# Optimization experiments

Hardware: AMD Instinct MI355X
Metric: run time of the kernel (lower is better)

## Reference

```python
import jax, jax.numpy as jnp
import numpy as np

B, SQ, SKV, D, H, DH, P = 8, 2048, 2048, 1024, 8, 128, 1024
LN_EPS = 1e-3  # keras LayerNormalization default


def _glorot(key, shape):
    fan_in, fan_out = shape[-2], shape[-1]
    lim = np.sqrt(6.0 / (fan_in + fan_out))
    return jax.random.uniform(key, shape, jnp.float32, -lim, lim)


def _layernorm(x, gamma, beta, eps=LN_EPS):
    mu = jnp.mean(x, axis=-1, keepdims=True)
    var = jnp.mean(jnp.square(x - mu), axis=-1, keepdims=True)
    return (x - mu) * jax.lax.rsqrt(var + eps) * gamma + beta


def setup_inputs() -> dict:
    key = jax.random.key(0)
    ks = jax.random.split(key, 8)
    return {
        "query": jax.random.normal(ks[0], (B, SQ, D), jnp.float32),
        "value": jax.random.normal(ks[1], (B, SKV, D), jnp.float32),
        "W1": _glorot(ks[2], (H, D, DH)),   # per-head query proj (stacked)
        "W2": _glorot(ks[3], (H, D, DH)),   # per-head key proj
        "W3": _glorot(ks[4], (H, D, DH)),   # per-head value proj
        "Wp": _glorot(ks[5], (H * DH, P)),  # output projection
        "bp": jnp.zeros((P,), jnp.float32),
        "Wt": _glorot(ks[6], (P, P)),       # transform (relu FFN)
        "bt": jnp.zeros((P,), jnp.float32),
        "g1": jnp.ones((P,), jnp.float32),
        "b1": jnp.zeros((P,), jnp.float32),
        "g2": jnp.ones((P,), jnp.float32),
        "b2": jnp.zeros((P,), jnp.float32),
    }


def reference(query, value, W1, W2, W3, Wp, bp, Wt, bt, g1, b1, g2, b2):
    # batched multi-head attention (original loops over heads; math identical)
    q = jnp.einsum("bsd,hde->bhse", query, W1)   # [B,H,SQ,DH]
    k = jnp.einsum("btd,hde->bhte", value, W2)   # [B,H,SKV,DH]
    v = jnp.einsum("btd,hde->bhte", value, W3)   # [B,H,SKV,DH]
    scale = 1.0 / jnp.sqrt(jnp.asarray(DH, jnp.float32))
    scores = jnp.einsum("bhse,bhte->bhst", q, k) * scale
    attn = jax.nn.softmax(scores, axis=-1)
    ctx = jnp.einsum("bhst,bhte->bhse", attn, v)  # [B,H,SQ,DH]
    # concat heads along feature axis
    cat = ctx.transpose(0, 2, 1, 3).reshape(B, SQ, H * DH)
    # project + residual + layernorm (dropout inactive: rate=0 / inference)
    proj = cat @ Wp + bp + query
    proj = _layernorm(proj, g1, b1)
    # relu transform + residual + layernorm
    t = jax.nn.relu(proj @ Wt + bt) + proj
    return _layernorm(t, g2, b2)
```

## Files before the change

kernel.cpp:

```cpp
#include <hip/hip_runtime.h>
#include <hip/hip_bf16.h>


typedef __bf16 bf16x8 __attribute__((ext_vector_type(8)));
typedef float  f32x4  __attribute__((ext_vector_type(4)));
typedef float  f32x16 __attribute__((ext_vector_type(16)));
typedef unsigned u32x4 __attribute__((ext_vector_type(4)));

#define GLDS16(g, l)                                                         \
  __builtin_amdgcn_global_load_lds(                                          \
      (__attribute__((address_space(1))) void*)(g),                          \
      (__attribute__((address_space(3))) void*)(l), 16, 0, 0)

__device__ __forceinline__ unsigned short f2bfu(float f) {
  unsigned int u = __builtin_bit_cast(unsigned int, f);
  u += 0x7fffu + ((u >> 16) & 1u);
  return (unsigned short)(u >> 16);
}
__device__ __forceinline__ float bfu2f(unsigned short u) {
  return __builtin_bit_cast(float, (unsigned int)u << 16);
}

__global__ __launch_bounds__(256) void cast2_f32_bf16(
    const float* __restrict__ in0, unsigned short* __restrict__ out0,
    const float* __restrict__ in1, unsigned short* __restrict__ out1, int n) {
  const float* in = blockIdx.z ? in1 : in0;
  unsigned short* out = blockIdx.z ? out1 : out0;
  int i = (blockIdx.x * 256 + threadIdx.x) * 4;
  int stride = gridDim.x * 256 * 4;
  for (; i < n; i += stride) {
    float4 v = *(const float4*)(in + i);
    ushort4 o;
    o.x = f2bfu(v.x); o.y = f2bfu(v.y); o.z = f2bfu(v.z); o.w = f2bfu(v.w);
    *(ushort4*)(out + i) = o;
  }
}

__device__ __forceinline__ void tc_body(const float* in, unsigned short* out,
                                        int R, int C) {
  __shared__ float tile[32][33];
  int tx = threadIdx.x, ty = threadIdx.y;
  int c0 = blockIdx.x * 32, r0 = blockIdx.y * 32;
#pragma unroll
  for (int j = 0; j < 4; j++)
    tile[ty + j * 8][tx] = in[(size_t)(r0 + ty + j * 8) * C + c0 + tx];
  __syncthreads();
#pragma unroll
  for (int j = 0; j < 4; j++)
    out[(size_t)(c0 + ty + j * 8) * R + r0 + tx] = f2bfu(tile[tx][ty + j * 8]);
}

__global__ __launch_bounds__(256) void transpose_heads(
    const float* __restrict__ W1, const float* __restrict__ W2,
    const float* __restrict__ W3, unsigned short* __restrict__ O1,
    unsigned short* __restrict__ O2, unsigned short* __restrict__ O3) {
  int z = blockIdx.z, t = z >> 3, s = z & 7;
  const float* in = (t == 0 ? W1 : t == 1 ? W2 : W3) + (size_t)s * 1024 * 128;
  unsigned short* out = (t == 0 ? O1 : t == 1 ? O2 : O3) + (size_t)s * 1024 * 128;
  tc_body(in, out, 1024, 128);
}

__global__ __launch_bounds__(256) void transpose_sq(
    const float* __restrict__ Wp, const float* __restrict__ Wt,
    unsigned short* __restrict__ Op, unsigned short* __restrict__ Ot) {
  const float* in = blockIdx.z ? Wt : Wp;
  unsigned short* out = blockIdx.z ? Ot : Op;
  tc_body(in, out, 1024, 1024);
}

template <int MODE>
__global__ __launch_bounds__(512, 2) void gemm256(
    const unsigned short* __restrict__ A, const unsigned short* __restrict__ Bt,
    void* __restrict__ out, const float* __restrict__ bias,
    const void* __restrict__ extra, float scale, float scale1,
    long strideA, long strideB, long strideO, int ntiles) {
  int bz = blockIdx.z;
  A  += (size_t)bz * strideA;
  Bt += (size_t)bz * strideB;
  float sc = bz ? scale1 : scale;
  int nb = gridDim.x;
  int qq = nb >> 3;
  int lin = blockIdx.x;
  int sw = (lin & 7) * qq + (lin >> 3);
  int nt = sw % ntiles, mt = sw / ntiles;
  int m0 = mt * 256, n0 = nt * 256;
  int tid = threadIdx.x;
  int wid = tid >> 6, lane = tid & 63;
  int l15 = lane & 15, l4 = lane >> 4;
  int wm = (wid >> 2) * 128, wn = (wid & 3) * 64;

  __shared__ alignas(16) char lds[131072];

  f32x4 acc[8][4];
#pragma unroll
  for (int i = 0; i < 8; i++)
#pragma unroll
    for (int j = 0; j < 4; j++) acc[i][j] = (f32x4){0.f, 0.f, 0.f, 0.f};

  const char* gA = (const char*)A + (size_t)m0 * 2048;
  const char* gB = (const char*)Bt + (size_t)n0 * 2048;

  auto STAGE = [&](int buf, int t) {
    char* ab = lds + buf * 65536;
    char* bb = ab + 32768;
#pragma unroll
    for (int i = 0; i < 4; i++) {
      int s = i * 512 + tid;
      int row = s >> 3;
      int g = (s & 7) ^ (row & 7);
      unsigned dst = (unsigned)((i * 512 + (tid & ~63)) * 16);
      GLDS16(gA + (size_t)row * 2048 + t * 128 + g * 16, ab + dst);
      GLDS16(gB + (size_t)row * 2048 + t * 128 + g * 16, bb + dst);
    }
  };

  STAGE(0, 0);
  for (int t = 0; t < 16; t++) {
    __builtin_amdgcn_sched_barrier(0);
    __builtin_amdgcn_s_barrier();
    if (t < 15) {
      STAGE((t + 1) & 1, t + 1);
      asm volatile("s_waitcnt vmcnt(8)" ::: "memory");
    } else {
      asm volatile("s_waitcnt vmcnt(0)" ::: "memory");
    }
    __builtin_amdgcn_s_barrier();
    __builtin_amdgcn_sched_barrier(0);

    const char* ab = lds + (t & 1) * 65536;
    const char* bb = ab + 32768;
#pragma unroll
    for (int kk = 0; kk < 2; kk++) {
      bf16x8 bfr[4];
#pragma unroll
      for (int nf = 0; nf < 4; nf++) {
        int r = wn + nf * 16 + l15;
        bfr[nf] = *(const bf16x8*)(bb + r * 128 + (((kk * 4 + l4) ^ (r & 7)) << 4));
      }
#pragma unroll
      for (int mh = 0; mh < 2; mh++) {
        bf16x8 af[4];
#pragma unroll
        for (int mf = 0; mf < 4; mf++) {
          int r = wm + mh * 64 + mf * 16 + l15;
          af[mf] = *(const bf16x8*)(ab + r * 128 + (((kk * 4 + l4) ^ (r & 7)) << 4));
        }
        __builtin_amdgcn_s_setprio(1);
#pragma unroll
        for (int mf = 0; mf < 4; mf++)
#pragma unroll
          for (int nf = 0; nf < 4; nf++)
            acc[mh * 4 + mf][nf] = __builtin_amdgcn_mfma_f32_16x16x32_bf16(
                af[mf], bfr[nf], acc[mh * 4 + mf][nf], 0, 0, 0);
        __builtin_amdgcn_s_setprio(0);
      }
    }
  }

  unsigned short* outp = (unsigned short*)out + (size_t)bz * strideO;
#pragma unroll
  for (int mi = 0; mi < 8; mi++)
#pragma unroll
    for (int nf = 0; nf < 4; nf++)
#pragma unroll
      for (int r = 0; r < 4; r++) {
        int gm = m0 + wm + mi * 16 + l4 * 4 + r;
        int gn = n0 + wn + nf * 16 + l15;
        float v = acc[mi][nf][r];
        if constexpr (MODE == 0) {
          int b = gm >> 11, s = gm & 2047, h = gn >> 7, e = gn & 127;
          outp[((((size_t)b * 8 + h) * 2048 + s) << 7) + e] = f2bfu(v * sc);
        } else if constexpr (MODE == 1) {
          outp[(size_t)gm * 2048 + gn] = f2bfu(v);
        } else if constexpr (MODE == 2) {
          float pl = bfu2f(((const unsigned short*)extra)[(size_t)gm * 1024 + gn]);
          outp[(size_t)gm * 1024 + gn] = f2bfu(v + bias[gn] + pl);
        } else {
          float pl = bfu2f(((const unsigned short*)extra)[(size_t)gm * 1024 + gn]);
          outp[(size_t)gm * 1024 + gn] = f2bfu(fmaxf(v + bias[gn], 0.0f) + pl);
        }
      }
}

__global__ __launch_bounds__(512) void fa_kernel(
    const unsigned short* __restrict__ Qh,
    const unsigned short* __restrict__ Kh,
    const unsigned short* __restrict__ Vt,
    unsigned short* __restrict__ catO) {
  int h = blockIdx.x, qt = blockIdx.y, b = blockIdx.z;
  int tid = threadIdx.x, wid = tid >> 6, lane = tid & 63;
  int q31 = lane & 31, hi = lane >> 5;

  __shared__ alignas(16) char lds[131072];

  const char* gK = (const char*)(Kh + (((size_t)b * 8 + h) * 2048) * 128);
  const char* gV = (const char*)(Vt + ((size_t)b * 1024 + h * 128) * 2048);

  bf16x8 qf[8];
  {
    const char* gQ = (const char*)(Qh + (((size_t)b * 8 + h) * 2048
                        + (size_t)qt * 256 + wid * 32 + q31) * 128);
#pragma unroll
    for (int ks = 0; ks < 8; ks++)
      qf[ks] = *(const bf16x8*)(gQ + ks * 32 + hi * 16);
  }

  f32x16 o[4];
#pragma unroll
  for (int et = 0; et < 4; et++)
#pragma unroll
    for (int r = 0; r < 16; r++) o[et][r] = 0.f;
  float lacc0 = 0.f, lacc1 = 0.f;

  auto STAGE_K = [&](int kt) {
    char* kb = lds + (kt & 3) * 16384;
#pragma unroll
    for (int pass = 0; pass < 2; pass++) {
      int c = pass * 512 + tid;
      int row = c >> 4, ch = c & 15;
      int g = ch ^ (row & 15);
      GLDS16(gK + (size_t)(kt * 64 + row) * 256 + g * 16,
             kb + (pass * 512 + (tid & ~63)) * 16);
    }
  };
  auto STAGE_V = [&](int kt) {
    char* vb = lds + 65536 + (kt & 3) * 16384;
#pragma unroll
    for (int pass = 0; pass < 2; pass++) {
      int c = pass * 512 + tid;
      int row = c >> 4, g = c & 15;
      int gp = g ^ (row & 15);
      int e = ((gp >> 3) << 6) + row;
      GLDS16(gV + (size_t)e * 4096 + kt * 128 + (gp & 7) * 16,
             vb + (pass * 512 + (tid & ~63)) * 16);
    }
  };
  auto QK = [&](int kt, f32x16& r0, f32x16& r1) {
    const char* kb = lds + (kt & 3) * 16384;
#pragma unroll
    for (int r = 0; r < 16; r++) { r0[r] = 0.f; r1[r] = 0.f; }
#pragma unroll
    for (int ks = 0; ks < 8; ks++) {
      int g = ((2 * ks + hi) ^ (q31 & 15)) << 4;
      bf16x8 k0 = *(const bf16x8*)(kb + q31 * 256 + g);
      bf16x8 k1 = *(const bf16x8*)(kb + (q31 + 32) * 256 + g);
      r0 = __builtin_amdgcn_mfma_f32_32x32x16_bf16(k0, qf[ks], r0, 0, 0, 0);
      r1 = __builtin_amdgcn_mfma_f32_32x32x16_bf16(k1, qf[ks], r1, 0, 0, 0);
    }
  };
  auto SOFT_PV = [&](int kt, f32x16& s0, f32x16& s1) {
    float p[32];
#pragma unroll
    for (int r = 0; r < 16; r++) p[r] = __builtin_amdgcn_exp2f(s0[r]);
#pragma unroll
    for (int r = 0; r < 16; r++) p[16 + r] = __builtin_amdgcn_exp2f(s1[r]);
#pragma unroll
    for (int r = 0; r < 16; r++) { lacc0 += p[r]; lacc1 += p[16 + r]; }
    bf16x8 pa[4];
#pragma unroll
    for (int g = 0; g < 4; g++) {
      unsigned a0, a1, b0, b1;
      float p0 = p[g * 8 + 0], p1 = p[g * 8 + 1], p2 = p[g * 8 + 2], p3 = p[g * 8 + 3];
      float p4 = p[g * 8 + 4], p5 = p[g * 8 + 5], p6 = p[g * 8 + 6], p7 = p[g * 8 + 7];
      asm("v_cvt_pk_bf16_f32 %0, %1, %2" : "=v"(a0) : "v"(p0), "v"(p1));
      asm("v_cvt_pk_bf16_f32 %0, %1, %2" : "=v"(b0) : "v"(p4), "v"(p5));
      asm("v_cvt_pk_bf16_f32 %0, %1, %2" : "=v"(a1) : "v"(p2), "v"(p3));
      asm("v_cvt_pk_bf16_f32 %0, %1, %2" : "=v"(b1) : "v"(p6), "v"(p7));
      asm volatile("v_permlane32_swap_b32 %0, %1" : "+v"(a0), "+v"(b0));
      asm volatile("v_permlane32_swap_b32 %0, %1" : "+v"(a1), "+v"(b1));
      u32x4 w; w[0] = a0; w[1] = a1; w[2] = b0; w[3] = b1;
      pa[g] = __builtin_bit_cast(bf16x8, w);
    }
    const char* vb = lds + 65536 + (kt & 3) * 16384;
#pragma unroll
    for (int et = 0; et < 4; et++) {
      int row = (et & 1) * 32 + q31;
      int gb = (et >> 1) * 8;
#pragma unroll
      for (int ks = 0; ks < 4; ks++) {
        bf16x8 vf = *(const bf16x8*)(vb + row * 256 +
                        (((gb + 2 * ks + hi) ^ (row & 15)) << 4));
        o[et] = __builtin_amdgcn_mfma_f32_32x32x16_bf16(vf, pa[ks], o[et], 0, 0, 0);
      }
    }
  };

  STAGE_K(0); STAGE_V(0); STAGE_K(1); STAGE_V(1);

  for (int w = 0; w < 16; w++) {
    int kt = 2 * w;
    asm volatile("s_waitcnt lgkmcnt(0)" ::: "memory");
    __builtin_amdgcn_sched_barrier(0);
    __builtin_amdgcn_s_barrier();
    if (w < 15) {
      STAGE_K(kt + 2); STAGE_V(kt + 2); STAGE_K(kt + 3); STAGE_V(kt + 3);
      asm volatile("s_waitcnt vmcnt(8)" ::: "memory");
    } else {
      asm volatile("s_waitcnt vmcnt(0)" ::: "memory");
    }
    __builtin_amdgcn_s_barrier();
    __builtin_amdgcn_sched_barrier(0);
    f32x16 sA0, sA1, sB0, sB1;
    QK(kt, sA0, sA1);
    QK(kt + 1, sB0, sB1);
    SOFT_PV(kt, sA0, sA1);
    SOFT_PV(kt + 1, sB0, sB1);
  }

  float lacc = lacc0 + lacc1;
  lacc += __shfl_xor(lacc, 32);
  float linv = 1.0f / lacc;
  __syncthreads();
  char* reg = lds + wid * 8192;
  int swz = (lane & 7) << 4;
#pragma unroll
  for (int et = 0; et < 4; et++)
#pragma unroll
    for (int pr = 0; pr < 8; pr++) {
      float lo = o[et][2 * pr] * linv, hf = o[et][2 * pr + 1] * linv;
      unsigned w;
      asm("v_cvt_pk_bf16_f32 %0, %1, %2" : "=v"(w) : "v"(lo), "v"(hf));
      int e = et * 32 + 8 * (pr >> 1) + 4 * hi + (pr & 1) * 2;
      *(unsigned*)(reg + q31 * 256 + ((e * 2) ^ swz)) = w;
    }
  size_t orow = (size_t)b * 2048 + (size_t)qt * 256 + wid * 32;
#pragma unroll
  for (int pass = 0; pass < 8; pass++) {
    int n = pass * 64 + lane;
    int q = n >> 4, ch = n & 15;
    bf16x8 v = *(const bf16x8*)(reg + q * 256 + ((ch * 16) ^ ((q & 7) << 4)));
    *(bf16x8*)((char*)(catO + (orow + q) * 1024 + h * 128) + ch * 16) = v;
  }
}

template <int IN_BF16, int OUT_BF16>
__global__ __launch_bounds__(256) void ln_kernel(
    const void* __restrict__ in, const float* __restrict__ g,
    const float* __restrict__ be, void* __restrict__ out) {
  int row = blockIdx.x;
  int tid = threadIdx.x;
  float4 v;
  if constexpr (IN_BF16) {
    ushort4 u = ((const ushort4*)in)[(size_t)row * 256 + tid];
    v.x = bfu2f(u.x); v.y = bfu2f(u.y); v.z = bfu2f(u.z); v.w = bfu2f(u.w);
  } else {
    v = ((const float4*)in)[(size_t)row * 256 + tid];
  }
  float s = v.x + v.y + v.z + v.w;
  float sq = v.x * v.x + v.y * v.y + v.z * v.z + v.w * v.w;
#pragma unroll
  for (int m = 1; m < 64; m <<= 1) {
    s += __shfl_xor(s, m);
    sq += __shfl_xor(sq, m);
  }
  __shared__ float ws[8];
  int wid = tid >> 6, lane = tid & 63;
  if (lane == 0) { ws[wid] = s; ws[wid + 4] = sq; }
  __syncthreads();
  s = ws[0] + ws[1] + ws[2] + ws[3];
  sq = ws[4] + ws[5] + ws[6] + ws[7];
  float mu = s * (1.0f / 1024.0f);
  float var = sq * (1.0f / 1024.0f) - mu * mu;
  float rs = rsqrtf(var + 1e-3f);
  float4 gg = ((const float4*)g)[tid];
  float4 bb = ((const float4*)be)[tid];
  float y0 = (v.x - mu) * rs * gg.x + bb.x;
  float y1 = (v.y - mu) * rs * gg.y + bb.y;
  float y2 = (v.z - mu) * rs * gg.z + bb.z;
  float y3 = (v.w - mu) * rs * gg.w + bb.w;
  if constexpr (OUT_BF16) {
    ushort4 ov;
    ov.x = f2bfu(y0); ov.y = f2bfu(y1); ov.z = f2bfu(y2); ov.w = f2bfu(y3);
    ((ushort4*)out)[(size_t)row * 256 + tid] = ov;
  } else {
    float4 ov = {y0, y1, y2, y3};
    ((float4*)out)[(size_t)row * 256 + tid] = ov;
  }
}

extern "C" void kernel_launch(void* const* d_in, const int* in_sizes, int n_in,
                              void* d_out, int out_size, void* d_ws, size_t ws_size,
                              hipStream_t stream) {
  const float* query = (const float*)d_in[0];
  const float* value = (const float*)d_in[1];
  const float* W1 = (const float*)d_in[2];
  const float* W2 = (const float*)d_in[3];
  const float* W3 = (const float*)d_in[4];
  const float* Wp = (const float*)d_in[5];
  const float* bp = (const float*)d_in[6];
  const float* Wt = (const float*)d_in[7];
  const float* bt = (const float*)d_in[8];
  const float* g1 = (const float*)d_in[9];
  const float* b1 = (const float*)d_in[10];
  const float* g2 = (const float*)d_in[11];
  const float* b2 = (const float*)d_in[12];

  char* ws = (char*)d_ws;
  unsigned short* qbf  = (unsigned short*)(ws + 0);
  unsigned short* vbf  = (unsigned short*)(ws + 33554432);
  unsigned short* Qh   = (unsigned short*)(ws + 67108864);
  unsigned short* Kh   = (unsigned short*)(ws + 100663296);
  unsigned short* Vt   = (unsigned short*)(ws + 134217728);
  unsigned short* Wq_t = (unsigned short*)(ws + 167772160);
  unsigned short* Wk_t = (unsigned short*)(ws + 169869312);
  unsigned short* Wv_t = (unsigned short*)(ws + 171966464);
  unsigned short* Wp_t = (unsigned short*)(ws + 174063616);
  unsigned short* Wt_t = (unsigned short*)(ws + 176160768);
  unsigned short* cat_  = vbf;
  unsigned short* projb = Qh;
  unsigned short* pln   = vbf;
  unsigned short* tb    = Kh;

  const int NE = 16384 * 1024;
  cast2_f32_bf16<<<dim3(2048, 1, 2), 256, 0, stream>>>(query, qbf, value, vbf, NE);

  dim3 tbk(32, 8);
  transpose_heads<<<dim3(4, 32, 24), tbk, 0, stream>>>(W1, W2, W3, Wq_t, Wk_t, Wv_t);
  transpose_sq<<<dim3(32, 32, 2), tbk, 0, stream>>>(Wp, Wt, Wp_t, Wt_t);

  const float QSCALE = 0.08838834764831845f * 1.4426950408889634f;
  gemm256<0><<<dim3(256, 1, 2), 512, 0, stream>>>(
      qbf, Wq_t, Qh, nullptr, nullptr, QSCALE, 1.0f,
      16777216L, 1048576L, 16777216L, 4);
  gemm256<1><<<dim3(32, 1, 8), 512, 0, stream>>>(
      Wv_t, vbf, Vt, nullptr, nullptr, 1.0f, 1.0f,
      0, 2048L * 1024L, 1024L * 2048L, 8);
  fa_kernel<<<dim3(8, 8, 8), 512, 0, stream>>>(Qh, Kh, Vt, cat_);
  gemm256<2><<<dim3(256, 1, 1), 512, 0, stream>>>(
      cat_, Wp_t, projb, bp, qbf, 1.0f, 1.0f, 0, 0, 0, 4);
  ln_kernel<1, 1><<<16384, 256, 0, stream>>>(projb, g1, b1, pln);
  gemm256<3><<<dim3(256, 1, 1), 512, 0, stream>>>(
      pln, Wt_t, tb, bt, pln, 1.0f, 1.0f, 0, 0, 0, 4);
  ln_kernel<1, 0><<<16384, 256, 0, stream>>>(tb, g2, b2, (float*)d_out);
}
```

Before: 399.8 us.

## Switch GEMMs to 128x128 tiles and fuse QKV projections into one launch

Replaces the 256x256, 512-thread GEMM with a 128x128, 256-thread core using 64KB of LDS. The Q, K and V projections now run in a single launch with per-block mode dispatch, and the two weight-transpose kernels are merged into one. The goal is more blocks per CU, better occupancy on a wider grid, and fewer launches. The cost is lower data reuse per tile, which means more global and LDS traffic per flop.

```diff
diff --git a/kernel.cpp b/kernel.cpp
--- a/kernel.cpp
+++ b/kernel.cpp
@@ -50,65 +50,41 @@
     out[(size_t)(c0 + ty + j * 8) * R + r0 + tx] = f2bfu(tile[tx][ty + j * 8]);
 }
 
-__global__ __launch_bounds__(256) void transpose_heads(
+__global__ __launch_bounds__(256) void transpose_all(
     const float* __restrict__ W1, const float* __restrict__ W2,
-    const float* __restrict__ W3, unsigned short* __restrict__ O1,
-    unsigned short* __restrict__ O2, unsigned short* __restrict__ O3) {
-  int z = blockIdx.z, t = z >> 3, s = z & 7;
-  const float* in = (t == 0 ? W1 : t == 1 ? W2 : W3) + (size_t)s * 1024 * 128;
-  unsigned short* out = (t == 0 ? O1 : t == 1 ? O2 : O3) + (size_t)s * 1024 * 128;
-  tc_body(in, out, 1024, 128);
-}
-
-__global__ __launch_bounds__(256) void transpose_sq(
-    const float* __restrict__ Wp, const float* __restrict__ Wt,
+    const float* __restrict__ W3, const float* __restrict__ Wp,
+    const float* __restrict__ Wt, unsigned short* __restrict__ O1,
+    unsigned short* __restrict__ O2, unsigned short* __restrict__ O3,
     unsigned short* __restrict__ Op, unsigned short* __restrict__ Ot) {
-  const float* in = blockIdx.z ? Wt : Wp;
-  unsigned short* out = blockIdx.z ? Ot : Op;
-  tc_body(in, out, 1024, 1024);
-}
-
-template <int MODE>
-__global__ __launch_bounds__(512, 2) void gemm256(
-    const unsigned short* __restrict__ A, const unsigned short* __restrict__ Bt,
-    void* __restrict__ out, const float* __restrict__ bias,
-    const void* __restrict__ extra, float scale, float scale1,
-    long strideA, long strideB, long strideO, int ntiles) {
-  int bz = blockIdx.z;
-  A  += (size_t)bz * strideA;
-  Bt += (size_t)bz * strideB;
-  float sc = bz ? scale1 : scale;
-  int nb = gridDim.x;
-  int qq = nb >> 3;
-  int lin = blockIdx.x;
-  int sw = (lin & 7) * qq + (lin >> 3);
-  int nt = sw % ntiles, mt = sw / ntiles;
-  int m0 = mt * 256, n0 = nt * 256;
-  int tid = threadIdx.x;
+  int z = blockIdx.z;
+  if (z < 24) {
+    if (blockIdx.x >= 4) return;
+    int t = z >> 3, s = z & 7;
+    const float* in = (t == 0 ? W1 : t == 1 ? W2 : W3) + (size_t)s * 1024 * 128;
+    unsigned short* out = (t == 0 ? O1 : t == 1 ? O2 : O3) + (size_t)s * 1024 * 128;
+    tc_body(in, out, 1024, 128);
+  } else {
+    const float* in = (z == 24) ? Wp : Wt;
+    unsigned short* out = (z == 24) ? Op : Ot;
+    tc_body(in, out, 1024, 1024);
+  }
+}
+
+__device__ __forceinline__ void gemm128_core(
+    const char* gA, const char* gB, char* lds, f32x4 (&acc)[4][4], int tid) {
   int wid = tid >> 6, lane = tid & 63;
   int l15 = lane & 15, l4 = lane >> 4;
-  int wm = (wid >> 2) * 128, wn = (wid & 3) * 64;
-
-  __shared__ alignas(16) char lds[131072];
-
-  f32x4 acc[8][4];
-#pragma unroll
-  for (int i = 0; i < 8; i++)
-#pragma unroll
-    for (int j = 0; j < 4; j++) acc[i][j] = (f32x4){0.f, 0.f, 0.f, 0.f};
-
-  const char* gA = (const char*)A + (size_t)m0 * 2048;
-  const char* gB = (const char*)Bt + (size_t)n0 * 2048;
+  int wm = (wid >> 1) * 64, wn = (wid & 1) * 64;
 
   auto STAGE = [&](int buf, int t) {
-    char* ab = lds + buf * 65536;
-    char* bb = ab + 32768;
+    char* ab = lds + buf * 32768;
+    char* bb = ab + 16384;
 #pragma unroll
     for (int i = 0; i < 4; i++) {
-      int s = i * 512 + tid;
+      int s = i * 256 + tid;
       int row = s >> 3;
       int g = (s & 7) ^ (row & 7);
-      unsigned dst = (unsigned)((i * 512 + (tid & ~63)) * 16);
+      unsigned dst = (unsigned)((i * 256 + (tid & ~63)) * 16);
       GLDS16(gA + (size_t)row * 2048 + t * 128 + g * 16, ab + dst);
       GLDS16(gB + (size_t)row * 2048 + t * 128 + g * 16, bb + dst);
     }
@@ -127,58 +103,133 @@
     __builtin_amdgcn_s_barrier();
     __builtin_amdgcn_sched_barrier(0);
 
-    const char* ab = lds + (t & 1) * 65536;
-    const char* bb = ab + 32768;
+    const char* ab = lds + (t & 1) * 32768;
+    const char* bb = ab + 16384;
 #pragma unroll
     for (int kk = 0; kk < 2; kk++) {
-      bf16x8 bfr[4];
-#pragma unroll
-      for (int nf = 0; nf < 4; nf++) {
-        int r = wn + nf * 16 + l15;
-        bfr[nf] = *(const bf16x8*)(bb + r * 128 + (((kk * 4 + l4) ^ (r & 7)) << 4));
+      bf16x8 af[4], bfr[4];
+#pragma unroll
+      for (int f = 0; f < 4; f++) {
+        int ra = wm + f * 16 + l15;
+        af[f] = *(const bf16x8*)(ab + ra * 128 + (((kk * 4 + l4) ^ (ra & 7)) << 4));
+        int rb = wn + f * 16 + l15;
+        bfr[f] = *(const bf16x8*)(bb + rb * 128 + (((kk * 4 + l4) ^ (rb & 7)) << 4));
       }
-#pragma unroll
-      for (int mh = 0; mh < 2; mh++) {
-        bf16x8 af[4];
-#pragma unroll
-        for (int mf = 0; mf < 4; mf++) {
-          int r = wm + mh * 64 + mf * 16 + l15;
-          af[mf] = *(const bf16x8*)(ab + r * 128 + (((kk * 4 + l4) ^ (r & 7)) << 4));
-        }
-        __builtin_amdgcn_s_setprio(1);
-#pragma unroll
-        for (int mf = 0; mf < 4; mf++)
-#pragma unroll
-          for (int nf = 0; nf < 4; nf++)
-            acc[mh * 4 + mf][nf] = __builtin_amdgcn_mfma_f32_16x16x32_bf16(
-                af[mf], bfr[nf], acc[mh * 4 + mf][nf], 0, 0, 0);
-        __builtin_amdgcn_s_setprio(0);
-      }
-    }
-  }
-
-  unsigned short* outp = (unsigned short*)out + (size_t)bz * strideO;
-#pragma unroll
-  for (int mi = 0; mi < 8; mi++)
+      __builtin_amdgcn_s_setprio(1);
+#pragma unroll
+      for (int mf = 0; mf < 4; mf++)
+#pragma unroll
+        for (int nf = 0; nf < 4; nf++)
+          acc[mf][nf] = __builtin_amdgcn_mfma_f32_16x16x32_bf16(
+              af[mf], bfr[nf], acc[mf][nf], 0, 0, 0);
+      __builtin_amdgcn_s_setprio(0);
+    }
+  }
+}
+
+__global__ __launch_bounds__(256, 2) void gemm_qkv(
+    const unsigned short* __restrict__ qbf, const unsigned short* __restrict__ vbf,
+    const unsigned short* __restrict__ Wq_t, const unsigned short* __restrict__ Wk_t,
+    const unsigned short* __restrict__ Wv_t, unsigned short* __restrict__ Qh,
+    unsigned short* __restrict__ Kh, unsigned short* __restrict__ Vt,
+    float qscale) {
+  int nb = gridDim.x;
+  int qq = nb >> 3;
+  int lin = blockIdx.x;
+  int idx = (lin & 7) * qq + (lin >> 3);
+
+  const unsigned short *A, *Bt;
+  unsigned short* outp;
+  int m0, n0, mode;
+  float sc = 1.0f;
+  if (idx < 2048) {
+    int seg = idx >> 10;
+    int t = idx & 1023;
+    m0 = (t >> 3) * 128; n0 = (t & 7) * 128;
+    A = seg ? vbf : qbf;
+    Bt = seg ? Wk_t : Wq_t;
+    outp = seg ? Kh : Qh;
+    if (!seg) sc = qscale;
+    mode = 0;
+  } else {
+    int v = idx - 2048;
+    int bz = v >> 7, t = v & 127;
+    m0 = (t >> 4) * 128; n0 = (t & 15) * 128;
+    A = Wv_t;
+    Bt = vbf + (size_t)bz * 2048 * 1024;
+    outp = Vt + (size_t)bz * 1024 * 2048;
+    mode = 1;
+  }
+
+  __shared__ alignas(16) char lds[65536];
+  f32x4 acc[4][4];
+#pragma unroll
+  for (int i = 0; i < 4; i++)
+#pragma unroll
+    for (int j = 0; j < 4; j++) acc[i][j] = (f32x4){0.f, 0.f, 0.f, 0.f};
+
+  gemm128_core((const char*)A + (size_t)m0 * 2048,
+               (const char*)Bt + (size_t)n0 * 2048, lds, acc, threadIdx.x);
+
+  int tid = threadIdx.x, wid = tid >> 6, lane = tid & 63;
+  int l15 = lane & 15, l4 = lane >> 4;
+  int wm = (wid >> 1) * 64, wn = (wid & 1) * 64;
+#pragma unroll
+  for (int mf = 0; mf < 4; mf++)
 #pragma unroll
     for (int nf = 0; nf < 4; nf++)
 #pragma unroll
       for (int r = 0; r < 4; r++) {
-        int gm = m0 + wm + mi * 16 + l4 * 4 + r;
+        int gm = m0 + wm + mf * 16 + l4 * 4 + r;
         int gn = n0 + wn + nf * 16 + l15;
-        float v = acc[mi][nf][r];
-        if constexpr (MODE == 0) {
+        float v = acc[mf][nf][r];
+        if (mode == 0) {
           int b = gm >> 11, s = gm & 2047, h = gn >> 7, e = gn & 127;
           outp[((((size_t)b * 8 + h) * 2048 + s) << 7) + e] = f2bfu(v * sc);
-        } else if constexpr (MODE == 1) {
+        } else {
           outp[(size_t)gm * 2048 + gn] = f2bfu(v);
-        } else if constexpr (MODE == 2) {
-          float pl = bfu2f(((const unsigned short*)extra)[(size_t)gm * 1024 + gn]);
-          outp[(size_t)gm * 1024 + gn] = f2bfu(v + bias[gn] + pl);
-        } else {
-          float pl = bfu2f(((const unsigned short*)extra)[(size_t)gm * 1024 + gn]);
-          outp[(size_t)gm * 1024 + gn] = f2bfu(fmaxf(v + bias[gn], 0.0f) + pl);
         }
+      }
+}
+
+template <int MODE>
+__global__ __launch_bounds__(256, 2) void gemm128_ep(
+    const unsigned short* __restrict__ A, const unsigned short* __restrict__ Bt,
+    unsigned short* __restrict__ out, const float* __restrict__ bias,
+    const unsigned short* __restrict__ extra) {
+  int nb = gridDim.x;
+  int qq = nb >> 3;
+  int lin = blockIdx.x;
+  int idx = (lin & 7) * qq + (lin >> 3);
+  int m0 = (idx >> 3) * 128, n0 = (idx & 7) * 128;
+
+  __shared__ alignas(16) char lds[65536];
+  f32x4 acc[4][4];
+#pragma unroll
+  for (int i = 0; i < 4; i++)
+#pragma unroll
+    for (int j = 0; j < 4; j++) acc[i][j] = (f32x4){0.f, 0.f, 0.f, 0.f};
+
+  gemm128_core((const char*)A + (size_t)m0 * 2048,
+               (const char*)Bt + (size_t)n0 * 2048, lds, acc, threadIdx.x);
+
+  int tid = threadIdx.x, wid = tid >> 6, lane = tid & 63;
+  int l15 = lane & 15, l4 = lane >> 4;
+  int wm = (wid >> 1) * 64, wn = (wid & 1) * 64;
+#pragma unroll
+  for (int mf = 0; mf < 4; mf++)
+#pragma unroll
+    for (int nf = 0; nf < 4; nf++)
+#pragma unroll
+      for (int r = 0; r < 4; r++) {
+        int gm = m0 + wm + mf * 16 + l4 * 4 + r;
+        int gn = n0 + wn + nf * 16 + l15;
+        float v = acc[mf][nf][r];
+        float pl = bfu2f(extra[(size_t)gm * 1024 + gn]);
+        if constexpr (MODE == 2)
+          out[(size_t)gm * 1024 + gn] = f2bfu(v + bias[gn] + pl);
+        else
+          out[(size_t)gm * 1024 + gn] = f2bfu(fmaxf(v + bias[gn], 0.0f) + pl);
       }
 }
 
@@ -414,22 +465,14 @@
   const int NE = 16384 * 1024;
   cast2_f32_bf16<<<dim3(2048, 1, 2), 256, 0, stream>>>(query, qbf, value, vbf, NE);
 
-  dim3 tbk(32, 8);
-  transpose_heads<<<dim3(4, 32, 24), tbk, 0, stream>>>(W1, W2, W3, Wq_t, Wk_t, Wv_t);
-  transpose_sq<<<dim3(32, 32, 2), tbk, 0, stream>>>(Wp, Wt, Wp_t, Wt_t);
+  transpose_all<<<dim3(32, 32, 26), dim3(32, 8), 0, stream>>>(
+      W1, W2, W3, Wp, Wt, Wq_t, Wk_t, Wv_t, Wp_t, Wt_t);
 
   const float QSCALE = 0.08838834764831845f * 1.4426950408889634f;
-  gemm256<0><<<dim3(256, 1, 2), 512, 0, stream>>>(
-      qbf, Wq_t, Qh, nullptr, nullptr, QSCALE, 1.0f,
-      16777216L, 1048576L, 16777216L, 4);
-  gemm256<1><<<dim3(32, 1, 8), 512, 0, stream>>>(
-      Wv_t, vbf, Vt, nullptr, nullptr, 1.0f, 1.0f,
-      0, 2048L * 1024L, 1024L * 2048L, 8);
+  gemm_qkv<<<3072, 256, 0, stream>>>(qbf, vbf, Wq_t, Wk_t, Wv_t, Qh, Kh, Vt, QSCALE);
   fa_kernel<<<dim3(8, 8, 8), 512, 0, stream>>>(Qh, Kh, Vt, cat_);
-  gemm256<2><<<dim3(256, 1, 1), 512, 0, stream>>>(
-      cat_, Wp_t, projb, bp, qbf, 1.0f, 1.0f, 0, 0, 0, 4);
+  gemm128_ep<2><<<1024, 256, 0, stream>>>(cat_, Wp_t, projb, bp, qbf);
   ln_kernel<1, 1><<<16384, 256, 0, stream>>>(projb, g1, b1, pln);
-  gemm256<3><<<dim3(256, 1, 1), 512, 0, stream>>>(
-      pln, Wt_t, tb, bt, pln, 1.0f, 1.0f, 0, 0, 0, 4);
+  gemm128_ep<3><<<1024, 256, 0, stream>>>(pln, Wt_t, tb, bt, pln);
   ln_kernel<1, 0><<<16384, 256, 0, stream>>>(tb, g2, b2, (float*)d_out);
 }
```

After: 414.1 us. 1.04x slower.
